# Kernel optimization log

Measured on AMD Instinct MI355X. Metric: run time of the kernel, lower is better.

Reference implementation:

```python
import jax, jax.numpy as jnp
import numpy as np

FEAT = 64      # feature_dim
HEADS = 4      # n_head
LATENT = 256   # latent_dim
G = 128        # num graphs
NPG = 150      # nodes per graph (<=180 for one-hot positions)
N = G * NPG    # 19200 nodes
E = N * 12     # 230400 edges (excl. self loops)
POS = 180      # one-hot position classes
SLOPE = 0.2    # PyG GATConv leaky_relu negative slope


def gat_conv(x, src, dst, W, att_s, att_d, bias):
    """PyG GATConv (concat heads, self loops already appended to src/dst)."""
    n = x.shape[0]
    h = (x @ W).reshape(n, HEADS, FEAT)                 # [N,H,F]
    a_s = jnp.sum(h * att_s, axis=-1)                   # [N,H]
    a_d = jnp.sum(h * att_d, axis=-1)                   # [N,H]
    e = jax.nn.leaky_relu(a_s[src] + a_d[dst], SLOPE)   # [E,H] per-edge logits
    m = jax.ops.segment_max(e, dst, num_segments=n)     # segment softmax over dst
    ex = jnp.exp(e - m[dst])
    s = jax.ops.segment_sum(ex, dst, num_segments=n)
    alpha = ex / (s[dst] + 1e-16)
    out = jax.ops.segment_sum(h[src] * alpha[:, :, None], dst, num_segments=n)
    return out.reshape(n, HEADS * FEAT) + bias


def setup_inputs() -> dict:
    key = jax.random.key(0)
    ks = jax.random.split(key, 20)

    def p(k, shape, fan_in):
        return jax.random.normal(k, shape, jnp.float32) / np.sqrt(fan_in).astype(np.float32)

    z = jax.random.normal(ks[0], (G, LATENT), jnp.float32)
    src = jax.random.randint(ks[1], (E,), 0, N, jnp.int32)
    dst = (src + jax.random.randint(ks[2], (E,), 1, N, jnp.int32)) % N  # no self loops
    edge_index = jnp.stack([src, dst])
    batch = jnp.repeat(jnp.arange(G, dtype=jnp.int32), NPG)

    in1 = FEAT + POS
    in2 = FEAT * HEADS
    inp = dict(z=z, edge_index=edge_index, batch=batch, num_graphs=G)
    inp.update(
        W0=p(ks[3], (LATENT, FEAT), LATENT), b0=jnp.zeros(FEAT, jnp.float32),
        W1=p(ks[4], (in1, HEADS * FEAT), in1),
        as1=p(ks[5], (HEADS, FEAT), FEAT), ad1=p(ks[6], (HEADS, FEAT), FEAT),
        bb1=jnp.zeros(HEADS * FEAT, jnp.float32),
        W2=p(ks[7], (in2, HEADS * FEAT), in2),
        as2=p(ks[8], (HEADS, FEAT), FEAT), ad2=p(ks[9], (HEADS, FEAT), FEAT),
        bb2=jnp.zeros(HEADS * FEAT, jnp.float32),
        W3=p(ks[10], (in2, HEADS * FEAT), in2),
        as3=p(ks[11], (HEADS, FEAT), FEAT), ad3=p(ks[12], (HEADS, FEAT), FEAT),
        bb3=jnp.zeros(HEADS * FEAT, jnp.float32),
        Wg=p(ks[13], (in2, FEAT), in2), bg=jnp.zeros(FEAT, jnp.float32),
        Wf=p(ks[14], (FEAT, 5), FEAT), bf=jnp.zeros(5, jnp.float32),
    )
    return inp


def reference(z, edge_index, batch, num_graphs,
              W0, b0, W1, as1, ad1, bb1, W2, as2, ad2, bb2,
              W3, as3, ad3, bb3, Wg, bg, Wf, bf):
    n = batch.shape[0]
    x = z @ W0 + b0                                    # dec_feature_init
    x = x[batch]                                       # broadcast graph latent to nodes
    # node_order_within_batch (batch is sorted)
    counts = jax.ops.segment_sum(jnp.ones_like(batch), batch, num_segments=num_graphs)
    starts = jnp.cumsum(counts) - counts
    order = jnp.arange(n, dtype=batch.dtype) - starts[batch]
    pos = jax.nn.one_hot(order, POS, dtype=x.dtype)
    x = jax.nn.relu(jnp.concatenate([x, pos], axis=1))
    # GATConv adds self loops by default
    loops = jnp.arange(n, dtype=edge_index.dtype)
    src = jnp.concatenate([edge_index[0], loops])
    dst = jnp.concatenate([edge_index[1], loops])
    x = jax.nn.relu(gat_conv(x, src, dst, W1, as1, ad1, bb1))
    x = jax.nn.relu(gat_conv(x, src, dst, W2, as2, ad2, bb2))
    x = jax.nn.relu(gat_conv(x, src, dst, W3, as3, ad3, bb3))
    x = jax.nn.relu(x @ Wg + bg)                       # dec_geo
    return x @ Wf + bf                                 # fc_geo -> [N,5]
```

## Files before the change

kernel.cpp:

```cpp
#include <hip/hip_runtime.h>
#include <hip/hip_fp16.h>

#define GNUM 128
#define HEADS 4
#define FEAT 64
#define CH 256
#define LAT 256
#define SLOPE 0.2f
#define CAP 64

typedef _Float16 h16;
typedef __attribute__((ext_vector_type(8))) _Float16 half8;
typedef __attribute__((ext_vector_type(4))) float floatx4;

__device__ __forceinline__ float lrelu(float x) { return fmaxf(x, SLOPE * x); }

__global__ void k_init(int* __restrict__ cnt, int n) {
  int i = blockIdx.x * blockDim.x + threadIdx.x;
  if (i < n) cnt[i] = 0;
}

__global__ void k_starts(const int* __restrict__ batch, int* __restrict__ starts, int n) {
  int i = blockIdx.x * blockDim.x + threadIdx.x;
  if (i < n) {
    int b = batch[i];
    if (i == 0 || batch[i - 1] != b) starts[b] = i;
  }
}

__global__ __launch_bounds__(256) void k_xzr(const float* __restrict__ z, const float* __restrict__ W0,
                                             const float* __restrict__ b0, float* __restrict__ xzr) {
  __shared__ float red[4][FEAT];
  int g = blockIdx.x, t = threadIdx.x;
  int f = t & 63, kq = t >> 6;
  float acc = 0.f;
  for (int k = kq * 64; k < kq * 64 + 64; ++k) acc += z[g * LAT + k] * W0[k * FEAT + f];
  red[kq][f] = acc;
  __syncthreads();
  if (kq == 0)
    xzr[g * FEAT + f] = fmaxf(red[0][f] + red[1][f] + red[2][f] + red[3][f] + b0[f], 0.f);
}

__global__ __launch_bounds__(256) void k_A(const float* __restrict__ xzr, const float* __restrict__ W1,
                                           float* __restrict__ A) {
  int g = blockIdx.x, c = threadIdx.x;
  float acc = 0.f;
  for (int k = 0; k < FEAT; ++k) acc += xzr[g * FEAT + k] * W1[k * CH + c];
  A[g * CH + c] = acc;
}

__global__ __launch_bounds__(256) void k_H1(const float* __restrict__ A, const float* __restrict__ W1,
                                            const int* __restrict__ batch, const int* __restrict__ starts,
                                            const float* __restrict__ att_s, const float* __restrict__ att_d,
                                            h16* __restrict__ H16, float* __restrict__ a_s,
                                            float* __restrict__ a_d) {
  int n = blockIdx.x, c = threadIdx.x;
  int g = batch[n];
  int p = n - starts[g];
  float val = A[g * CH + c] + W1[(FEAT + p) * CH + c];
  H16[(size_t)n * CH + c] = (h16)val;
  float ps = val * att_s[c];
  float pd = val * att_d[c];
#pragma unroll
  for (int w = 1; w < 64; w <<= 1) {
    ps += __shfl_xor(ps, w, 64);
    pd += __shfl_xor(pd, w, 64);
  }
  if ((c & 63) == 0) {
    int h = c >> 6;
    a_s[n * 4 + h] = ps;
    a_d[n * 4 + h] = pd;
  }
}

__global__ void k_w16(const float* __restrict__ W2, const float* __restrict__ W3,
                      const float* __restrict__ Wg, h16* __restrict__ W2T,
                      h16* __restrict__ W3T, h16* __restrict__ WgT) {
  int idx = blockIdx.x * 256 + threadIdx.x;
  if (idx < 65536) {
    int kb = idx >> 13, rem = idx & 8191, j = rem >> 8, nn = rem & 255;
    W2T[kb * 8192 + nn * 32 + j] = (h16)W2[(kb * 32 + j) * 256 + nn];
  } else if (idx < 131072) {
    int l = idx - 65536;
    int kb = l >> 13, rem = l & 8191, j = rem >> 8, nn = rem & 255;
    W3T[kb * 8192 + nn * 32 + j] = (h16)W3[(kb * 32 + j) * 256 + nn];
  } else if (idx < 147456) {
    int l = idx - 131072;
    int kb = l >> 11, rem = l & 2047, j = rem >> 6, nn = rem & 63;
    WgT[kb * 2048 + nn * 32 + j] = (h16)Wg[(kb * 32 + j) * 64 + nn];
  }
}

__global__ void k_scatter(const int* __restrict__ src, const int* __restrict__ dst,
                          int* __restrict__ cnt, int* __restrict__ bucket, int e) {
  int i = blockIdx.x * blockDim.x + threadIdx.x;
  if (i < e) {
    int d = dst[i];
    int p = atomicAdd(&cnt[d], 1);
    if (p < CAP) bucket[d * CAP + p] = src[i];
  }
}

__global__ __launch_bounds__(256) void k_galpha(const h16* __restrict__ H16, const float* __restrict__ a_s,
                                                const float* __restrict__ a_d, const float* __restrict__ bias,
                                                const int* __restrict__ cnt, const int* __restrict__ bucket,
                                                h16* __restrict__ X16) {
  __shared__ float wsh[4][CAP][4];
  __shared__ int bsh[4][CAP];
  int wv = threadIdx.x >> 6, lane = threadIdx.x & 63;
  int n = blockIdx.x * 4 + wv;
  int c = min(cnt[n], CAP);
  bool valid = lane < c;
  int sc = valid ? bucket[n * CAP + lane] : n;
  if (valid) bsh[wv][lane] = sc;
  float4 ea4 = *(const float4*)(a_s + (size_t)sc * 4);
  float4 sn4 = *(const float4*)(a_s + (size_t)n * 4);
  float4 dn4 = *(const float4*)(a_d + (size_t)n * 4);
  float ea[4] = {ea4.x, ea4.y, ea4.z, ea4.w};
  float sn[4] = {sn4.x, sn4.y, sn4.z, sn4.w};
  float dn[4] = {dn4.x, dn4.y, dn4.z, dn4.w};
  float asf[4];
#pragma unroll
  for (int h = 0; h < 4; ++h) {
    float e = valid ? lrelu(ea[h] + dn[h]) : -1e30f;
    float es = lrelu(sn[h] + dn[h]);
    float m = e;
#pragma unroll
    for (int sh = 1; sh < 64; sh <<= 1) m = fmaxf(m, __shfl_xor(m, sh, 64));
    m = fmaxf(m, es);
    float wgt = valid ? __expf(e - m) : 0.f;
    float ws = __expf(es - m);
    float s = wgt;
#pragma unroll
    for (int sh = 1; sh < 64; sh <<= 1) s += __shfl_xor(s, sh, 64);
    s += ws;
    float inv = 1.f / (s + 1e-16f);
    if (valid) wsh[wv][lane][h] = wgt * inv;
    asf[h] = ws * inv;
  }
  __syncthreads();
  const h16* hn = H16 + (size_t)n * CH;
  float acc0 = asf[0] * (float)hn[0 * FEAT + lane];
  float acc1 = asf[1] * (float)hn[1 * FEAT + lane];
  float acc2 = asf[2] * (float)hn[2 * FEAT + lane];
  float acc3 = asf[3] * (float)hn[3 * FEAT + lane];
  for (int j = 0; j < c; ++j) {
    int s2 = bsh[wv][j];
    const h16* hs = H16 + (size_t)s2 * CH;
    float4 wj = *(const float4*)&wsh[wv][j][0];
    acc0 += wj.x * (float)hs[0 * FEAT + lane];
    acc1 += wj.y * (float)hs[1 * FEAT + lane];
    acc2 += wj.z * (float)hs[2 * FEAT + lane];
    acc3 += wj.w * (float)hs[3 * FEAT + lane];
  }
  h16* xo = X16 + (size_t)n * CH;
  xo[0 * FEAT + lane] = (h16)fmaxf(acc0 + bias[0 * FEAT + lane], 0.f);
  xo[1 * FEAT + lane] = (h16)fmaxf(acc1 + bias[1 * FEAT + lane], 0.f);
  xo[2 * FEAT + lane] = (h16)fmaxf(acc2 + bias[2 * FEAT + lane], 0.f);
  xo[3 * FEAT + lane] = (h16)fmaxf(acc3 + bias[3 * FEAT + lane], 0.f);
}

__global__ __launch_bounds__(256) void k_gemm(const h16* __restrict__ X16, const h16* __restrict__ WT,
                                              const float* __restrict__ att_s, const float* __restrict__ att_d,
                                              h16* __restrict__ H16, float* __restrict__ a_s,
                                              float* __restrict__ a_d) {
  __shared__ h16 As[64 * 40];
  __shared__ h16 Bs[256 * 40];
  __shared__ h16 Ht[64 * 264];
  int t = threadIdx.x;
  int w = t >> 6, lane = t & 63;
  int quad = lane >> 4, l15 = lane & 15;
  int row0 = blockIdx.x * 64;
  floatx4 acc[4][4];
#pragma unroll
  for (int i = 0; i < 4; ++i)
#pragma unroll
    for (int j = 0; j < 4; ++j) acc[i][j] = (floatx4){0.f, 0.f, 0.f, 0.f};
  int srow = t >> 2, sseg = t & 3;
  for (int kb = 0; kb < 8; ++kb) {
    __syncthreads();
    *(half8*)&As[srow * 40 + sseg * 8] =
        *(const half8*)(X16 + (size_t)(row0 + srow) * CH + kb * 32 + sseg * 8);
    {
      const h16* src = WT + kb * 8192 + t * 32;
      h16* dst = &Bs[t * 40];
      *(half8*)(dst + 0)  = *(const half8*)(src + 0);
      *(half8*)(dst + 8)  = *(const half8*)(src + 8);
      *(half8*)(dst + 16) = *(const half8*)(src + 16);
      *(half8*)(dst + 24) = *(const half8*)(src + 24);
    }
    __syncthreads();
    half8 af[4], bf[4];
#pragma unroll
    for (int mt = 0; mt < 4; ++mt) af[mt] = *(const half8*)&As[(mt * 16 + l15) * 40 + quad * 8];
#pragma unroll
    for (int nt = 0; nt < 4; ++nt)
      bf[nt] = *(const half8*)&Bs[(w * 64 + nt * 16 + l15) * 40 + quad * 8];
#pragma unroll
    for (int mt = 0; mt < 4; ++mt)
#pragma unroll
      for (int nt = 0; nt < 4; ++nt)
        acc[mt][nt] = __builtin_amdgcn_mfma_f32_16x16x32_f16(af[mt], bf[nt], acc[mt][nt], 0, 0, 0);
  }
  __syncthreads();
#pragma unroll
  for (int mt = 0; mt < 4; ++mt)
#pragma unroll
    for (int nt = 0; nt < 4; ++nt)
#pragma unroll
      for (int r = 0; r < 4; ++r)
        Ht[(mt * 16 + quad * 4 + r) * 264 + w * 64 + nt * 16 + l15] = (h16)acc[mt][nt][r];
  float asv[4], adv[4];
#pragma unroll
  for (int nt = 0; nt < 4; ++nt) {
    asv[nt] = att_s[w * FEAT + nt * 16 + l15];
    adv[nt] = att_d[w * FEAT + nt * 16 + l15];
  }
#pragma unroll
  for (int mt = 0; mt < 4; ++mt)
#pragma unroll
    for (int r = 0; r < 4; ++r) {
      float ps = acc[mt][0][r] * asv[0] + acc[mt][1][r] * asv[1] +
                 acc[mt][2][r] * asv[2] + acc[mt][3][r] * asv[3];
      float pd = acc[mt][0][r] * adv[0] + acc[mt][1][r] * adv[1] +
                 acc[mt][2][r] * adv[2] + acc[mt][3][r] * adv[3];
#pragma unroll
      for (int sh = 1; sh < 16; sh <<= 1) {
        ps += __shfl_xor(ps, sh, 16);
        pd += __shfl_xor(pd, sh, 16);
      }
      if (l15 == 0) {
        int row = row0 + mt * 16 + quad * 4 + r;
        a_s[row * 4 + w] = ps;
        a_d[row * 4 + w] = pd;
      }
    }
  __syncthreads();
  {
    const h16* srcr = &Ht[srow * 264 + sseg * 64];
    h16* dstr = H16 + (size_t)(row0 + srow) * CH + sseg * 64;
#pragma unroll
    for (int i = 0; i < 8; ++i) *(half8*)(dstr + i * 8) = *(const half8*)(srcr + i * 8);
  }
}

__global__ __launch_bounds__(256) void k_head(const h16* __restrict__ X16, const h16* __restrict__ WgT,
                                              const float* __restrict__ bg, const float* __restrict__ Wf,
                                              const float* __restrict__ bfv, float* __restrict__ out) {
  __shared__ h16 As[64 * 40];
  __shared__ h16 Bs[64 * 40];
  __shared__ float ytile[64 * 68];
  __shared__ float WfS[FEAT * 5];
  int t = threadIdx.x;
  int w = t >> 6, lane = t & 63;
  int quad = lane >> 4, l15 = lane & 15;
  int row0 = blockIdx.x * 64;
  for (int i = t; i < FEAT * 5; i += 256) WfS[i] = Wf[i];
  floatx4 acc[4];
#pragma unroll
  for (int mt = 0; mt < 4; ++mt) acc[mt] = (floatx4){0.f, 0.f, 0.f, 0.f};
  int srow = t >> 2, sseg = t & 3;
  for (int kb = 0; kb < 8; ++kb) {
    __syncthreads();
    *(half8*)&As[srow * 40 + sseg * 8] =
        *(const half8*)(X16 + (size_t)(row0 + srow) * CH + kb * 32 + sseg * 8);
    *(half8*)&Bs[srow * 40 + sseg * 8] =
        *(const half8*)(WgT + kb * 2048 + srow * 32 + sseg * 8);
    __syncthreads();
    half8 af[4], bf;
#pragma unroll
    for (int mt = 0; mt < 4; ++mt) af[mt] = *(const half8*)&As[(mt * 16 + l15) * 40 + quad * 8];
    bf = *(const half8*)&Bs[(w * 16 + l15) * 40 + quad * 8];
#pragma unroll
    for (int mt = 0; mt < 4; ++mt)
      acc[mt] = __builtin_amdgcn_mfma_f32_16x16x32_f16(af[mt], bf, acc[mt], 0, 0, 0);
  }
  __syncthreads();
  int col = w * 16 + l15;
  float bgv = bg[col];
#pragma unroll
  for (int mt = 0; mt < 4; ++mt)
#pragma unroll
    for (int r = 0; r < 4; ++r)
      ytile[(mt * 16 + quad * 4 + r) * 68 + col] = fmaxf(acc[mt][r] + bgv, 0.f);
  __syncthreads();
  for (int i = t; i < 64 * 5; i += 256) {
    int row = i / 5, o = i % 5;
    float s = bfv[o];
#pragma unroll
    for (int k = 0; k < FEAT; ++k) s += ytile[row * 68 + k] * WfS[k * 5 + o];
    out[(size_t)(row0 + row) * 5 + o] = s;
  }
}

static inline size_t alignup(size_t x) { return (x + 255) & ~(size_t)255; }

extern "C" void kernel_launch(void* const* d_in, const int* in_sizes, int n_in,
                              void* d_out, int out_size, void* d_ws, size_t ws_size,
                              hipStream_t stream) {
  (void)n_in; (void)out_size; (void)ws_size;
  const float* z   = (const float*)d_in[0];
  const int* edge  = (const int*)d_in[1];
  const int* batch = (const int*)d_in[2];
  const float* W0  = (const float*)d_in[4];
  const float* b0  = (const float*)d_in[5];
  const float* W1  = (const float*)d_in[6];
  const float* as1 = (const float*)d_in[7];
  const float* ad1 = (const float*)d_in[8];
  const float* bb1 = (const float*)d_in[9];
  const float* W2  = (const float*)d_in[10];
  const float* as2 = (const float*)d_in[11];
  const float* ad2 = (const float*)d_in[12];
  const float* bb2 = (const float*)d_in[13];
  const float* W3  = (const float*)d_in[14];
  const float* as3 = (const float*)d_in[15];
  const float* ad3 = (const float*)d_in[16];
  const float* bb3 = (const float*)d_in[17];
  const float* Wg  = (const float*)d_in[18];
  const float* bg  = (const float*)d_in[19];
  const float* Wf  = (const float*)d_in[20];
  const float* bfv = (const float*)d_in[21];
  float* out = (float*)d_out;

  const int E = in_sizes[1] / 2;
  const int N = in_sizes[2];
  const int* srcI = edge;
  const int* dstI = edge + E;

  char* w = (char*)d_ws;
  auto carve = [&](size_t bytes) { void* p = (void*)w; w += alignup(bytes); return p; };
  int* starts  = (int*)carve((size_t)GNUM * 4);
  int* cnt     = (int*)carve((size_t)N * 4);
  int* bucket  = (int*)carve((size_t)N * CAP * 4);
  float* xzr   = (float*)carve((size_t)GNUM * FEAT * 4);
  float* A     = (float*)carve((size_t)GNUM * CH * 4);
  float* a_s   = (float*)carve((size_t)N * 4 * 4);
  float* a_d   = (float*)carve((size_t)N * 4 * 4);
  h16* W2T     = (h16*)carve((size_t)CH * CH * 2);
  h16* W3T     = (h16*)carve((size_t)CH * CH * 2);
  h16* WgT     = (h16*)carve((size_t)CH * FEAT * 2);
  h16* H16     = (h16*)carve((size_t)N * CH * 2);
  h16* X16     = (h16*)carve((size_t)N * CH * 2);

  int nb256 = (N + 255) / 256;
  int eb256 = (E + 255) / 256;

  hipLaunchKernelGGL(k_init, dim3(nb256), dim3(256), 0, stream, cnt, N);
  hipLaunchKernelGGL(k_starts, dim3(nb256), dim3(256), 0, stream, batch, starts, N);
  hipLaunchKernelGGL(k_w16, dim3(576), dim3(256), 0, stream, W2, W3, Wg, W2T, W3T, WgT);
  hipLaunchKernelGGL(k_xzr, dim3(GNUM), dim3(256), 0, stream, z, W0, b0, xzr);
  hipLaunchKernelGGL(k_A, dim3(GNUM), dim3(256), 0, stream, xzr, W1, A);
  hipLaunchKernelGGL(k_H1, dim3(N), dim3(256), 0, stream, A, W1, batch, starts, as1, ad1, H16, a_s, a_d);
  hipLaunchKernelGGL(k_scatter, dim3(eb256), dim3(256), 0, stream, srcI, dstI, cnt, bucket, E);

  hipLaunchKernelGGL(k_galpha, dim3(N / 4), dim3(256), 0, stream, H16, a_s, a_d, bb1, cnt, bucket, X16);
  hipLaunchKernelGGL(k_gemm, dim3(N / 64), dim3(256), 0, stream, X16, W2T, as2, ad2, H16, a_s, a_d);
  hipLaunchKernelGGL(k_galpha, dim3(N / 4), dim3(256), 0, stream, H16, a_s, a_d, bb2, cnt, bucket, X16);
  hipLaunchKernelGGL(k_gemm, dim3(N / 64), dim3(256), 0, stream, X16, W3T, as3, ad3, H16, a_s, a_d);
  hipLaunchKernelGGL(k_galpha, dim3(N / 4), dim3(256), 0, stream, H16, a_s, a_d, bb3, cnt, bucket, X16);
  hipLaunchKernelGGL(k_head, dim3(N / 64), dim3(256), 0, stream, X16, WgT, bg, Wf, bfv, out);
}
```

Baseline: 281.4 us.

## Remap aggregation to one node per block, merge tiny kernels, alias shared memory

The attention-aggregation kernel now assigns one destination node per 256-thread block, with one wavefront per head and one column per thread, where before each wave handled a whole node across all four heads. This raises parallelism and cuts per-thread serial work, at the cost of four times as many blocks and redundant neighbour-index loads. The init and starts kernels are merged into one, as are the latent projection and the first-layer A computation, removing launches and an intermediate buffer. The GEMM and head kernels now alias their staging and output tiles in shared memory to lower LDS usage and improve occupancy.

```diff
diff --git a/kernel.cpp b/kernel.cpp
--- a/kernel.cpp
+++ b/kernel.cpp
@@ -15,22 +15,21 @@
 
 __device__ __forceinline__ float lrelu(float x) { return fmaxf(x, SLOPE * x); }
 
-__global__ void k_init(int* __restrict__ cnt, int n) {
-  int i = blockIdx.x * blockDim.x + threadIdx.x;
-  if (i < n) cnt[i] = 0;
-}
-
-__global__ void k_starts(const int* __restrict__ batch, int* __restrict__ starts, int n) {
+__global__ void k_initstarts(const int* __restrict__ batch, int* __restrict__ cnt,
+                             int* __restrict__ starts, int n) {
   int i = blockIdx.x * blockDim.x + threadIdx.x;
   if (i < n) {
+    cnt[i] = 0;
     int b = batch[i];
     if (i == 0 || batch[i - 1] != b) starts[b] = i;
   }
 }
 
-__global__ __launch_bounds__(256) void k_xzr(const float* __restrict__ z, const float* __restrict__ W0,
-                                             const float* __restrict__ b0, float* __restrict__ xzr) {
+__global__ __launch_bounds__(256) void k_xzrA(const float* __restrict__ z, const float* __restrict__ W0,
+                                              const float* __restrict__ b0, const float* __restrict__ W1,
+                                              float* __restrict__ A) {
   __shared__ float red[4][FEAT];
+  __shared__ float xzs[FEAT];
   int g = blockIdx.x, t = threadIdx.x;
   int f = t & 63, kq = t >> 6;
   float acc = 0.f;
@@ -38,15 +37,12 @@
   red[kq][f] = acc;
   __syncthreads();
   if (kq == 0)
-    xzr[g * FEAT + f] = fmaxf(red[0][f] + red[1][f] + red[2][f] + red[3][f] + b0[f], 0.f);
-}
-
-__global__ __launch_bounds__(256) void k_A(const float* __restrict__ xzr, const float* __restrict__ W1,
-                                           float* __restrict__ A) {
-  int g = blockIdx.x, c = threadIdx.x;
-  float acc = 0.f;
-  for (int k = 0; k < FEAT; ++k) acc += xzr[g * FEAT + k] * W1[k * CH + c];
-  A[g * CH + c] = acc;
+    xzs[f] = fmaxf(red[0][f] + red[1][f] + red[2][f] + red[3][f] + b0[f], 0.f);
+  __syncthreads();
+  float a2 = 0.f;
+#pragma unroll 16
+  for (int k = 0; k < FEAT; ++k) a2 += xzs[k] * W1[k * CH + t];
+  A[g * CH + t] = a2;
 }
 
 __global__ __launch_bounds__(256) void k_H1(const float* __restrict__ A, const float* __restrict__ W1,
@@ -105,68 +101,50 @@
                                                 const float* __restrict__ a_d, const float* __restrict__ bias,
                                                 const int* __restrict__ cnt, const int* __restrict__ bucket,
                                                 h16* __restrict__ X16) {
-  __shared__ float wsh[4][CAP][4];
-  __shared__ int bsh[4][CAP];
-  int wv = threadIdx.x >> 6, lane = threadIdx.x & 63;
-  int n = blockIdx.x * 4 + wv;
+  __shared__ int bsh[CAP];
+  __shared__ float wsh[4][CAP];
+  int t = threadIdx.x;
+  int w = t >> 6, lane = t & 63;
+  int n = blockIdx.x;
   int c = min(cnt[n], CAP);
   bool valid = lane < c;
   int sc = valid ? bucket[n * CAP + lane] : n;
-  if (valid) bsh[wv][lane] = sc;
-  float4 ea4 = *(const float4*)(a_s + (size_t)sc * 4);
-  float4 sn4 = *(const float4*)(a_s + (size_t)n * 4);
-  float4 dn4 = *(const float4*)(a_d + (size_t)n * 4);
-  float ea[4] = {ea4.x, ea4.y, ea4.z, ea4.w};
-  float sn[4] = {sn4.x, sn4.y, sn4.z, sn4.w};
-  float dn[4] = {dn4.x, dn4.y, dn4.z, dn4.w};
-  float asf[4];
-#pragma unroll
-  for (int h = 0; h < 4; ++h) {
-    float e = valid ? lrelu(ea[h] + dn[h]) : -1e30f;
-    float es = lrelu(sn[h] + dn[h]);
-    float m = e;
-#pragma unroll
-    for (int sh = 1; sh < 64; sh <<= 1) m = fmaxf(m, __shfl_xor(m, sh, 64));
-    m = fmaxf(m, es);
-    float wgt = valid ? __expf(e - m) : 0.f;
-    float ws = __expf(es - m);
-    float s = wgt;
-#pragma unroll
-    for (int sh = 1; sh < 64; sh <<= 1) s += __shfl_xor(s, sh, 64);
-    s += ws;
-    float inv = 1.f / (s + 1e-16f);
-    if (valid) wsh[wv][lane][h] = wgt * inv;
-    asf[h] = ws * inv;
-  }
-  __syncthreads();
-  const h16* hn = H16 + (size_t)n * CH;
-  float acc0 = asf[0] * (float)hn[0 * FEAT + lane];
-  float acc1 = asf[1] * (float)hn[1 * FEAT + lane];
-  float acc2 = asf[2] * (float)hn[2 * FEAT + lane];
-  float acc3 = asf[3] * (float)hn[3 * FEAT + lane];
+  if (w == 0 && valid) bsh[lane] = sc;
+  float dnw = a_d[n * 4 + w];
+  float snw = a_s[n * 4 + w];
+  float e = valid ? lrelu(a_s[sc * 4 + w] + dnw) : -1e30f;
+  float es = lrelu(snw + dnw);
+  float m = e;
+#pragma unroll
+  for (int sh = 1; sh < 64; sh <<= 1) m = fmaxf(m, __shfl_xor(m, sh, 64));
+  m = fmaxf(m, es);
+  float wgt = valid ? __expf(e - m) : 0.f;
+  float ws = __expf(es - m);
+  float s = wgt;
+#pragma unroll
+  for (int sh = 1; sh < 64; sh <<= 1) s += __shfl_xor(s, sh, 64);
+  s += ws;
+  float inv = 1.f / (s + 1e-16f);
+  if (valid) wsh[w][lane] = wgt * inv;
+  float asf = ws * inv;
+  __syncthreads();
+  int col = w * FEAT + lane;
+  float acc = asf * (float)H16[(size_t)n * CH + col];
   for (int j = 0; j < c; ++j) {
-    int s2 = bsh[wv][j];
-    const h16* hs = H16 + (size_t)s2 * CH;
-    float4 wj = *(const float4*)&wsh[wv][j][0];
-    acc0 += wj.x * (float)hs[0 * FEAT + lane];
-    acc1 += wj.y * (float)hs[1 * FEAT + lane];
-    acc2 += wj.z * (float)hs[2 * FEAT + lane];
-    acc3 += wj.w * (float)hs[3 * FEAT + lane];
-  }
-  h16* xo = X16 + (size_t)n * CH;
-  xo[0 * FEAT + lane] = (h16)fmaxf(acc0 + bias[0 * FEAT + lane], 0.f);
-  xo[1 * FEAT + lane] = (h16)fmaxf(acc1 + bias[1 * FEAT + lane], 0.f);
-  xo[2 * FEAT + lane] = (h16)fmaxf(acc2 + bias[2 * FEAT + lane], 0.f);
-  xo[3 * FEAT + lane] = (h16)fmaxf(acc3 + bias[3 * FEAT + lane], 0.f);
+    int s2 = bsh[j];
+    acc += wsh[w][j] * (float)H16[(size_t)s2 * CH + col];
+  }
+  X16[(size_t)n * CH + col] = (h16)fmaxf(acc + bias[col], 0.f);
 }
 
 __global__ __launch_bounds__(256) void k_gemm(const h16* __restrict__ X16, const h16* __restrict__ WT,
                                               const float* __restrict__ att_s, const float* __restrict__ att_d,
                                               h16* __restrict__ H16, float* __restrict__ a_s,
                                               float* __restrict__ a_d) {
-  __shared__ h16 As[64 * 40];
-  __shared__ h16 Bs[256 * 40];
-  __shared__ h16 Ht[64 * 264];
+  __shared__ __align__(16) char smem[64 * 264 * 2];
+  h16* As = (h16*)smem;
+  h16* Bs = (h16*)(smem + 64 * 40 * 2);
+  h16* Ht = (h16*)smem;
   int t = threadIdx.x;
   int w = t >> 6, lane = t & 63;
   int quad = lane >> 4, l15 = lane & 15;
@@ -247,9 +225,10 @@
 __global__ __launch_bounds__(256) void k_head(const h16* __restrict__ X16, const h16* __restrict__ WgT,
                                               const float* __restrict__ bg, const float* __restrict__ Wf,
                                               const float* __restrict__ bfv, float* __restrict__ out) {
-  __shared__ h16 As[64 * 40];
-  __shared__ h16 Bs[64 * 40];
-  __shared__ float ytile[64 * 68];
+  __shared__ __align__(16) char smem[64 * 68 * 4];
+  h16* As = (h16*)smem;
+  h16* Bs = (h16*)(smem + 64 * 40 * 2);
+  float* ytile = (float*)smem;
   __shared__ float WfS[FEAT * 5];
   int t = threadIdx.x;
   int w = t >> 6, lane = t & 63;
@@ -332,7 +311,6 @@
   int* starts  = (int*)carve((size_t)GNUM * 4);
   int* cnt     = (int*)carve((size_t)N * 4);
   int* bucket  = (int*)carve((size_t)N * CAP * 4);
-  float* xzr   = (float*)carve((size_t)GNUM * FEAT * 4);
   float* A     = (float*)carve((size_t)GNUM * CH * 4);
   float* a_s   = (float*)carve((size_t)N * 4 * 4);
   float* a_d   = (float*)carve((size_t)N * 4 * 4);
@@ -345,18 +323,16 @@
   int nb256 = (N + 255) / 256;
   int eb256 = (E + 255) / 256;
 
-  hipLaunchKernelGGL(k_init, dim3(nb256), dim3(256), 0, stream, cnt, N);
-  hipLaunchKernelGGL(k_starts, dim3(nb256), dim3(256), 0, stream, batch, starts, N);
+  hipLaunchKernelGGL(k_initstarts, dim3(nb256), dim3(256), 0, stream, batch, cnt, starts, N);
   hipLaunchKernelGGL(k_w16, dim3(576), dim3(256), 0, stream, W2, W3, Wg, W2T, W3T, WgT);
-  hipLaunchKernelGGL(k_xzr, dim3(GNUM), dim3(256), 0, stream, z, W0, b0, xzr);
-  hipLaunchKernelGGL(k_A, dim3(GNUM), dim3(256), 0, stream, xzr, W1, A);
+  hipLaunchKernelGGL(k_xzrA, dim3(GNUM), dim3(256), 0, stream, z, W0, b0, W1, A);
   hipLaunchKernelGGL(k_H1, dim3(N), dim3(256), 0, stream, A, W1, batch, starts, as1, ad1, H16, a_s, a_d);
   hipLaunchKernelGGL(k_scatter, dim3(eb256), dim3(256), 0, stream, srcI, dstI, cnt, bucket, E);
 
-  hipLaunchKernelGGL(k_galpha, dim3(N / 4), dim3(256), 0, stream, H16, a_s, a_d, bb1, cnt, bucket, X16);
+  hipLaunchKernelGGL(k_galpha, dim3(N), dim3(256), 0, stream, H16, a_s, a_d, bb1, cnt, bucket, X16);
   hipLaunchKernelGGL(k_gemm, dim3(N / 64), dim3(256), 0, stream, X16, W2T, as2, ad2, H16, a_s, a_d);
-  hipLaunchKernelGGL(k_galpha, dim3(N / 4), dim3(256), 0, stream, H16, a_s, a_d, bb2, cnt, bucket, X16);
+  hipLaunchKernelGGL(k_galpha, dim3(N), dim3(256), 0, stream, H16, a_s, a_d, bb2, cnt, bucket, X16);
   hipLaunchKernelGGL(k_gemm, dim3(N / 64), dim3(256), 0, stream, X16, W3T, as3, ad3, H16, a_s, a_d);
-  hipLaunchKernelGGL(k_galpha, dim3(N / 4), dim3(256), 0, stream, H16, a_s, a_d, bb3, cnt, bucket, X16);
+  hipLaunchKernelGGL(k_galpha, dim3(N), dim3(256), 0, stream, H16, a_s, a_d, bb3, cnt, bucket, X16);
   hipLaunchKernelGGL(k_head, dim3(N / 64), dim3(256), 0, stream, X16, WgT, bg, Wf, bfv, out);
 }
```

Measured after the change: 329.4 us. +17.1%, slower.
